# Kernel optimization log

Measured on AMD Instinct MI355X. Metric: run time of the kernel, lower is better.

## Reference

```python
import jax, jax.numpy as jnp
import numpy as np

NUM_TAGS = 19
START_ID = 17  # lbl_to_id['START_LBL']
PAD_ID = 18    # lbl_to_id['PAD_LBL']
NEG = -1000.0


def setup_inputs() -> dict:
    key = jax.random.key(0)
    k1, k2, k3 = jax.random.split(key, 3)
    B, L = 512, 2048
    P = jax.random.normal(k1, (B, L, NUM_TAGS), dtype=jnp.float32)
    T = jax.random.normal(k2, (NUM_TAGS, NUM_TAGS), dtype=jnp.float32)
    # contiguous-prefix valid mask, lengths in [1, L]
    lengths = jax.random.randint(k3, (B,), 1, L + 1)
    mask = jnp.arange(L)[None, :] < lengths[:, None]  # [B, L] bool
    return {"P": P, "T": T, "mask": mask}


def _viterbi_forward(P, T, mask):
    # P: [B, L, K] emissions; T[j, k] = score of transition prev=k -> cur=j
    B, L, K = P.shape
    DP0 = jnp.full((B, K), NEG, dtype=P.dtype).at[:, START_ID].set(0.0)

    def step(DP, xs):
        emit, m = xs  # emit: [B, K], m: [B] bool
        scores = DP[:, None, :] + T[None, :, :]        # [B, cur, prev]
        best = scores.max(axis=-1)                      # [B, K]
        arg = scores.argmax(axis=-1).astype(jnp.int32)  # [B, K] backpointers
        new_DP = best + emit
        DP = jnp.where(m[:, None], new_DP, DP)          # frozen past sequence end
        return DP, arg

    DP, choice = jax.lax.scan(
        step, DP0, (jnp.swapaxes(P, 0, 1), jnp.swapaxes(mask, 0, 1))
    )  # choice: [L, B, K]
    DP = DP + T[PAD_ID][None, :]  # transition into PAD at the end
    return DP, choice


def reference(P, T, mask):
    B, L, K = P.shape
    DP, choice = _viterbi_forward(P, T, mask)
    last = DP.argmax(axis=-1).astype(jnp.int32)          # [B] best final tag
    lengths = mask.sum(axis=-1).astype(jnp.int32)        # [B]
    bidx = jnp.arange(B)

    def back(c, t):
        # path[t] = choice[t+1][path[t+1]] for t < len-1; path[len-1] = last
        nxt = choice[jnp.minimum(t + 1, L - 1), bidx, c]  # [B]
        new_c = jnp.where(t < lengths - 1, nxt, c)
        out = jnp.where(t < lengths, new_c, -1)           # -1 pads beyond length
        return new_c, out

    _, outs = jax.lax.scan(back, last, jnp.arange(L - 1, -1, -1))  # [L, B]
    path = jnp.flip(jnp.swapaxes(outs, 0, 1), axis=1)  # [B, L], decoded tags
    return path
```

## Files before the change

kernel.cpp:

```cpp
#include <hip/hip_runtime.h>

#define Bn 512
#define Ln 2048
#define Kn 19
#define NEGV (-1000.0f)
#define START_IDn 17
#define PAD_IDn 18
#define SEG 64
#define PBYTES 79691776u


#define DP_CORE(BASE)                                                          \
    float4 q0 = *(const float4*)((BASE) + 0);                                  \
    float4 q1 = *(const float4*)((BASE) + 4);                                  \
    float4 q2 = *(const float4*)((BASE) + 8);                                  \
    float4 q3 = *(const float4*)((BASE) + 12);                                 \
    float4 q4 = *(const float4*)((BASE) + 16);            \
    float cand[Kn];                                                            \
    cand[0]  = q0.x + Trow[0];  cand[1]  = q0.y + Trow[1];                     \
    cand[2]  = q0.z + Trow[2];  cand[3]  = q0.w + Trow[3];                     \
    cand[4]  = q1.x + Trow[4];  cand[5]  = q1.y + Trow[5];                     \
    cand[6]  = q1.z + Trow[6];  cand[7]  = q1.w + Trow[7];                     \
    cand[8]  = q2.x + Trow[8];  cand[9]  = q2.y + Trow[9];                     \
    cand[10] = q2.z + Trow[10]; cand[11] = q2.w + Trow[11];                    \
    cand[12] = q3.x + Trow[12]; cand[13] = q3.y + Trow[13];                    \
    cand[14] = q3.z + Trow[14]; cand[15] = q3.w + Trow[15];                    \
    cand[16] = q4.x + Trow[16]; cand[17] = q4.y + Trow[17];                    \
    cand[18] = q4.z + Trow[18];                                                \
    float m0 = fmaxf(fmaxf(cand[0],  cand[1]),  cand[2]);                      \
    float m1 = fmaxf(fmaxf(cand[3],  cand[4]),  cand[5]);                      \
    float m2 = fmaxf(fmaxf(cand[6],  cand[7]),  cand[8]);                      \
    float m3 = fmaxf(fmaxf(cand[9],  cand[10]), cand[11]);                     \
    float m4 = fmaxf(fmaxf(cand[12], cand[13]), cand[14]);                     \
    float m5 = fmaxf(fmaxf(cand[15], cand[16]), cand[17]);                     \
    float n0 = fmaxf(fmaxf(m0, m1), m2);                                       \
    float n1 = fmaxf(fmaxf(m3, m4), cand[18]);                                 \
    float best = fmaxf(fmaxf(n0, n1), m5);

__global__ __launch_bounds__(64, 1) void crf_fwd(
    const float* __restrict__ P, const float* __restrict__ T,
    const int* __restrict__ mask, float* __restrict__ dpck,
    float* __restrict__ dpfin, int* __restrict__ lens)
{
    const int lane = threadIdx.x;
    const int half = lane >> 5;
    const int c = lane & 31;
    const int b = blockIdx.x * 2 + half;
    const int cc = (c < Kn) ? c : (Kn - 1);

    float Trow[Kn];
#pragma unroll
    for (int p = 0; p < Kn; ++p) Trow[p] = T[cc * Kn + p];

    const int* mrow = mask + (size_t)b * Ln;
    int sum = 0;
#pragma unroll
    for (int j = 0; j < Ln / 128; ++j) {
        int4 v = *(const int4*)(mrow + j * 128 + c * 4);
        sum += v.x + v.y + v.z + v.w;
    }
#pragma unroll
    for (int k = 1; k < 32; k <<= 1) sum += __shfl_xor(sum, k, 64);
    const int len = sum;
    if (c == 0) lens[b] = len;
    const int lenO = __shfl_xor(len, 32, 64);
    int maxlen = len > lenO ? len : lenO;
    int lmin = len < lenO ? len : lenO;
    lmin = __builtin_amdgcn_readfirstlane(lmin);
    int mlen = (maxlen + (SEG - 1)) & ~(SEG - 1);
    mlen = __builtin_amdgcn_readfirstlane(mlen);

    __shared__ float dp[2][32];
    __shared__ float ebuf[2][2][1280];

    float mydp = (c == START_IDn) ? 0.0f : NEGV;
    dp[half][c] = mydp;

    const unsigned bbyte = (unsigned)b * (Ln * Kn * 4u);
    const unsigned limit = PBYTES - 16;
    const char* Pc = (const char*)P;
    float4 r[10];

#define STAGE_LOAD(ci)                                                         \
    { unsigned base_ = bbyte + (unsigned)(ci) * 4864u + ((unsigned)c << 4);    \
      _Pragma("unroll")                                                        \
      for (int i_ = 0; i_ < 10; ++i_) {                                        \
          unsigned o_ = base_ + (unsigned)i_ * 512u;                           \
          if (o_ > limit) o_ = limit;                                          \
          r[i_] = *(const float4*)(Pc + o_);                                   \
      } }
#define STAGE_WRITE(nb)                                                        \
    { float* d_ = &ebuf[nb][half][(unsigned)c << 2];                           \
      _Pragma("unroll")                                                        \
      for (int i_ = 0; i_ < 10; ++i_) *(float4*)(d_ + i_ * 128) = r[i_]; }

    int buf = 0;
    STAGE_LOAD(0);
    STAGE_WRITE(0);

    for (int t0 = 0; t0 < mlen; t0 += SEG) {
        if (c < Kn)
            dpck[((unsigned)b * 32u + (unsigned)(t0 >> 6)) * (unsigned)Kn + (unsigned)c] = mydp;
        STAGE_LOAD((t0 >> 6) + 1);
        const float* ebl = &ebuf[buf][half][0];

        if (t0 + SEG <= lmin) {
            for (int tt = 0; tt < SEG; tt += 8) {
#pragma unroll
                for (int u = 0; u < 8; ++u) {
                    const float e = ebl[(tt + u) * Kn + cc];
                    const float* base_ = &dp[half][0];
                    DP_CORE(base_)
                    mydp = best + e;
                    dp[half][c] = mydp;
                }
            }
        } else {
            for (int tt = 0; tt < SEG; tt += 8) {
#pragma unroll
                for (int u = 0; u < 8; ++u) {
                    const int t = t0 + tt + u;
                    const float e = ebl[(tt + u) * Kn + cc];
                    const float* base_ = &dp[half][0];
                    DP_CORE(base_)
                    float nd = best + e;
                    mydp = (t < len) ? nd : mydp;
                    dp[half][c] = mydp;
                }
            }
        }
        STAGE_WRITE(buf ^ 1);
        buf ^= 1;
    }
    if (c < Kn) dpfin[b * Kn + c] = mydp;
#undef STAGE_LOAD
#undef STAGE_WRITE
}

__global__ __launch_bounds__(256) void crf_rec(
    const float* __restrict__ P, const float* __restrict__ T,
    const float* __restrict__ dpck, const int* __restrict__ lens,
    unsigned char* __restrict__ choice)
{
    const int tid = threadIdx.x;
    const int halfid = tid >> 5;
    const int c = tid & 31;
    const int cc = (c < Kn) ? c : (Kn - 1);
    const int task = blockIdx.x * 8 + halfid;
    const int b = task >> 5;
    const int seg = task & 31;
    const int t0 = seg * SEG;
    const int len = lens[b];
    if (t0 >= len) return;

    __shared__ float dp[8][32];
    __shared__ __align__(16) unsigned char cbuf[8][SEG * Kn];

    float Trow[Kn];
#pragma unroll
    for (int p = 0; p < Kn; ++p) Trow[p] = T[cc * Kn + p];

    float mydp = (c < Kn) ? dpck[((unsigned)b * 32u + (unsigned)seg) * (unsigned)Kn + (unsigned)c]
                          : NEGV;
    dp[halfid][c] = mydp;

    const float* prow = P + (size_t)b * Ln * Kn + (size_t)t0 * Kn;

    float eb[8];
#pragma unroll
    for (int u = 0; u < 8; ++u) eb[u] = prow[u * Kn + cc];

    for (int tt = 0; tt < SEG; tt += 8) {
#pragma unroll
        for (int u = 0; u < 8; ++u) {
            const int t = t0 + tt + u;
            const float e = eb[u];
            const float* base_ = &dp[halfid][0];
            DP_CORE(base_)
            float nd = best + e;
            mydp = (t < len) ? nd : mydp;
            dp[halfid][c] = mydp;

            int arg = Kn - 1;
#pragma unroll
            for (int p = Kn - 2; p >= 0; --p)
                arg = (cand[p] == best) ? p : arg;
            if (c < Kn) cbuf[halfid][(tt + u) * Kn + c] = (unsigned char)arg;

            int tn = tt + u + 8;
            int tloc = (t0 + tn < Ln) ? tn : (Ln - 1 - t0);
            eb[u] = prow[tloc * Kn + cc];
        }
    }
    {
        const int4* s = (const int4*)&cbuf[halfid][0];
        int4* d = (int4*)(choice + (size_t)b * Ln * Kn + (size_t)t0 * Kn);
        for (int i = c; i < (SEG * Kn) / 16; i += 32) d[i] = s[i];
    }
}

__global__ __launch_bounds__(384, 1) void crf_bwd(
    const float* __restrict__ T, const unsigned char* __restrict__ choice,
    const float* __restrict__ dpfin, const int* __restrict__ lens,
    int* __restrict__ out)
{
    __shared__ unsigned char comp[Ln * Kn];
    __shared__ int vchain[17];
    __shared__ int s_last, s_len;

    const int b = blockIdx.x;
    const int tid = threadIdx.x;

    {
        const int4* src = (const int4*)(choice + (size_t)b * Ln * Kn);
        int4* dst = (int4*)comp;
        for (int i = tid; i < (Ln * Kn) / 16; i += 384) dst[i] = src[i];
    }
    if (tid == 0) {
        s_len = lens[b];
        float bestv = dpfin[b * Kn + 0] + T[PAD_IDn * Kn + 0];
        int bl = 0;
        for (int ci = 1; ci < Kn; ++ci) {
            float v = dpfin[b * Kn + ci] + T[PAD_IDn * Kn + ci];
            if (v > bestv) { bestv = v; bl = ci; }
        }
        s_last = bl;
    }
    __syncthreads();
    const int len = s_len;

    {
        const int wv = tid >> 6;
        const int lane = tid & 63;
        const int ch = wv * 3 + lane / Kn;
        const int c = lane % Kn;
        if (lane < 3 * Kn && ch < 16) {
            int cur = c;
            const int tb = ch * 128 + 127;
            for (int i = 0; i < 128; ++i) {
                const int t = tb - i;
                int nv = comp[t * Kn + cur];
                cur = (t < len) ? nv : cur;
                comp[t * Kn + c] = cur;
            }
        }
    }
    __syncthreads();

    if (tid == 0) {
        int v = s_last;
        vchain[16] = v;
        for (int ch = 15; ch >= 0; --ch) {
            v = comp[ch * 128 * Kn + v];
            vchain[ch] = v;
        }
    }
    __syncthreads();

    const int last = s_last;
    int* orow = out + (size_t)b * Ln;
    for (int t = tid; t < Ln; t += 384) {
        int val;
        if (t >= len) {
            val = -1;
        } else if (t == Ln - 1) {
            val = last;
        } else {
            const int tp = t + 1;
            const int vc = vchain[(tp >> 7) + 1];
            val = comp[tp * Kn + vc];
        }
        orow[t] = val;
    }
}

extern "C" void kernel_launch(void* const* d_in, const int* in_sizes, int n_in,
                              void* d_out, int out_size, void* d_ws, size_t ws_size,
                              hipStream_t stream)
{
    const float* P    = (const float*)d_in[0];
    const float* T    = (const float*)d_in[1];
    const int*   mask = (const int*)d_in[2];
    int* out = (int*)d_out;

    const size_t choice_bytes = (size_t)Bn * Ln * Kn;
    unsigned char* choice = (unsigned char*)d_ws;
    float* dpfin = (float*)((char*)d_ws + choice_bytes);
    int* lens = (int*)((char*)d_ws + choice_bytes + (size_t)Bn * Kn * 4);

    float* dpck = (float*)((char*)d_out + 2 * 1024 * 1024);

    crf_fwd<<<Bn / 2, 64, 0, stream>>>(P, T, mask, dpck, dpfin, lens);
    crf_rec<<<(Bn * 32) / 8, 256, 0, stream>>>(P, T, dpck, lens, choice);
    crf_bwd<<<Bn, 384, 0, stream>>>(T, choice, dpfin, lens, out);
}
```

Baseline: 400.3 us.

## Fuse segment recompute and backtrack kernels, keeping backpointers in shared memory

Merges the per-segment recompute kernel and the backtrace kernel into one 1024-thread block per sequence. Backpointers are written directly into shared memory instead of a global choice buffer that was later reloaded, removing about 20 MB of global write and read traffic and one launch. The tradeoff is one block per sequence with large LDS use, which limits occupancy and ties the recompute parallelism to 512 blocks. The backtrack chunk mapping is changed to one wave per 128-step chunk.

New measurement: 393.5 us. About the same (-1.7%).

```diff
diff --git a/kernel.cpp b/kernel.cpp
--- a/kernel.cpp
+++ b/kernel.cpp
@@ -137,87 +137,65 @@
 #undef STAGE_WRITE
 }
 
-__global__ __launch_bounds__(256) void crf_rec(
+__global__ __launch_bounds__(1024, 1) void crf_recbwd(
     const float* __restrict__ P, const float* __restrict__ T,
-    const float* __restrict__ dpck, const int* __restrict__ lens,
-    unsigned char* __restrict__ choice)
+    const float* __restrict__ dpck, const float* __restrict__ dpfin,
+    const int* __restrict__ lens, int* __restrict__ out)
 {
+    const int b = blockIdx.x;
     const int tid = threadIdx.x;
     const int halfid = tid >> 5;
     const int c = tid & 31;
     const int cc = (c < Kn) ? c : (Kn - 1);
-    const int task = blockIdx.x * 8 + halfid;
-    const int b = task >> 5;
-    const int seg = task & 31;
-    const int t0 = seg * SEG;
+    const int t0 = halfid * SEG;
     const int len = lens[b];
-    if (t0 >= len) return;
-
-    __shared__ float dp[8][32];
-    __shared__ __align__(16) unsigned char cbuf[8][SEG * Kn];
-
-    float Trow[Kn];
-#pragma unroll
-    for (int p = 0; p < Kn; ++p) Trow[p] = T[cc * Kn + p];
-
-    float mydp = (c < Kn) ? dpck[((unsigned)b * 32u + (unsigned)seg) * (unsigned)Kn + (unsigned)c]
-                          : NEGV;
-    dp[halfid][c] = mydp;
-
-    const float* prow = P + (size_t)b * Ln * Kn + (size_t)t0 * Kn;
-
-    float eb[8];
-#pragma unroll
-    for (int u = 0; u < 8; ++u) eb[u] = prow[u * Kn + cc];
-
-    for (int tt = 0; tt < SEG; tt += 8) {
-#pragma unroll
-        for (int u = 0; u < 8; ++u) {
-            const int t = t0 + tt + u;
-            const float e = eb[u];
-            const float* base_ = &dp[halfid][0];
-            DP_CORE(base_)
-            float nd = best + e;
-            mydp = (t < len) ? nd : mydp;
-            dp[halfid][c] = mydp;
-
-            int arg = Kn - 1;
-#pragma unroll
-            for (int p = Kn - 2; p >= 0; --p)
-                arg = (cand[p] == best) ? p : arg;
-            if (c < Kn) cbuf[halfid][(tt + u) * Kn + c] = (unsigned char)arg;
-
-            int tn = tt + u + 8;
-            int tloc = (t0 + tn < Ln) ? tn : (Ln - 1 - t0);
-            eb[u] = prow[tloc * Kn + cc];
-        }
-    }
-    {
-        const int4* s = (const int4*)&cbuf[halfid][0];
-        int4* d = (int4*)(choice + (size_t)b * Ln * Kn + (size_t)t0 * Kn);
-        for (int i = c; i < (SEG * Kn) / 16; i += 32) d[i] = s[i];
-    }
-}
-
-__global__ __launch_bounds__(384, 1) void crf_bwd(
-    const float* __restrict__ T, const unsigned char* __restrict__ choice,
-    const float* __restrict__ dpfin, const int* __restrict__ lens,
-    int* __restrict__ out)
-{
+
     __shared__ unsigned char comp[Ln * Kn];
+    __shared__ float dp[32][32];
     __shared__ int vchain[17];
-    __shared__ int s_last, s_len;
-
-    const int b = blockIdx.x;
-    const int tid = threadIdx.x;
-
-    {
-        const int4* src = (const int4*)(choice + (size_t)b * Ln * Kn);
-        int4* dst = (int4*)comp;
-        for (int i = tid; i < (Ln * Kn) / 16; i += 384) dst[i] = src[i];
-    }
+    __shared__ int s_last;
+
+    if (t0 < len) {
+        float Trow[Kn];
+#pragma unroll
+        for (int p = 0; p < Kn; ++p) Trow[p] = T[cc * Kn + p];
+
+        float mydp = (c < Kn)
+            ? dpck[((unsigned)b * 32u + (unsigned)halfid) * (unsigned)Kn + (unsigned)c]
+            : NEGV;
+        dp[halfid][c] = mydp;
+
+        const float* prow = P + (size_t)b * Ln * Kn + (size_t)t0 * Kn;
+
+        float eb[8];
+#pragma unroll
+        for (int u = 0; u < 8; ++u) eb[u] = prow[u * Kn + cc];
+
+        for (int tt = 0; tt < SEG; tt += 8) {
+#pragma unroll
+            for (int u = 0; u < 8; ++u) {
+                const int t = t0 + tt + u;
+                const float e = eb[u];
+                const float* base_ = &dp[halfid][0];
+                DP_CORE(base_)
+                float nd = best + e;
+                mydp = (t < len) ? nd : mydp;
+                dp[halfid][c] = mydp;
+
+                int arg = Kn - 1;
+#pragma unroll
+                for (int p = Kn - 2; p >= 0; --p)
+                    arg = (cand[p] == best) ? p : arg;
+                if (c < Kn) comp[t * Kn + c] = (unsigned char)arg;
+
+                int tn = tt + u + 8;
+                int tloc = (t0 + tn < Ln) ? tn : (Ln - 1 - t0);
+                eb[u] = prow[tloc * Kn + cc];
+            }
+        }
+    }
+
     if (tid == 0) {
-        s_len = lens[b];
         float bestv = dpfin[b * Kn + 0] + T[PAD_IDn * Kn + 0];
         int bl = 0;
         for (int ci = 1; ci < Kn; ++ci) {
@@ -227,21 +205,18 @@
         s_last = bl;
     }
     __syncthreads();
-    const int len = s_len;
 
     {
         const int wv = tid >> 6;
-        const int lane = tid & 63;
-        const int ch = wv * 3 + lane / Kn;
-        const int c = lane % Kn;
-        if (lane < 3 * Kn && ch < 16) {
-            int cur = c;
-            const int tb = ch * 128 + 127;
+        const int lane2 = tid & 63;
+        if (lane2 < Kn) {
+            int cur = lane2;
+            const int tb = wv * 128 + 127;
             for (int i = 0; i < 128; ++i) {
                 const int t = tb - i;
                 int nv = comp[t * Kn + cur];
                 cur = (t < len) ? nv : cur;
-                comp[t * Kn + c] = cur;
+                comp[t * Kn + lane2] = cur;
             }
         }
     }
@@ -259,7 +234,7 @@
 
     const int last = s_last;
     int* orow = out + (size_t)b * Ln;
-    for (int t = tid; t < Ln; t += 384) {
+    for (int t = tid; t < Ln; t += 1024) {
         int val;
         if (t >= len) {
             val = -1;
@@ -284,13 +259,10 @@
     int* out = (int*)d_out;
 
     const size_t choice_bytes = (size_t)Bn * Ln * Kn;
-    unsigned char* choice = (unsigned char*)d_ws;
+    float* dpck  = (float*)d_ws;
     float* dpfin = (float*)((char*)d_ws + choice_bytes);
     int* lens = (int*)((char*)d_ws + choice_bytes + (size_t)Bn * Kn * 4);
 
-    float* dpck = (float*)((char*)d_out + 2 * 1024 * 1024);
-
     crf_fwd<<<Bn / 2, 64, 0, stream>>>(P, T, mask, dpck, dpfin, lens);
-    crf_rec<<<(Bn * 32) / 8, 256, 0, stream>>>(P, T, dpck, lens, choice);
-    crf_bwd<<<Bn, 384, 0, stream>>>(T, choice, dpfin, lens, out);
+    crf_recbwd<<<Bn, 1024, 0, stream>>>(P, T, dpck, dpfin, lens, out);
 }
```
